# Performance work log

Measured on AMD Instinct MI355X. Metric: run time of the kernel, lower is better.

## Reference

```python
import math
import jax, jax.numpy as jnp
import numpy as np

NEG_INF = -jnp.inf


def setup_inputs() -> dict:
    key = jax.random.key(0)
    k1, k2, k3 = jax.random.split(key, 3)
    B, T, D = 2, 2048, 1024
    x = jax.random.normal(k1, (B, T, D), dtype=jnp.float32)
    w_qkv = jax.random.normal(k2, (3 * D, D), dtype=jnp.float32) * (1.0 / math.sqrt(D))
    w_out = jax.random.normal(k3, (D, D), dtype=jnp.float32) * (1.0 / math.sqrt(D))
    return {"x": x, "w_qkv": w_qkv, "w_out": w_out, "n_heads": 16, "k": 8}


def reference(x, w_qkv, w_out, n_heads, k):
    B, T, D = x.shape
    head_dim = D // n_heads
    scale = math.sqrt(head_dim)

    qkv = x @ w_qkv.T                                   # (B,T,3D), torch Linear: x W^T
    q, kk, v = jnp.split(qkv, 3, axis=-1)

    def split_heads(t):
        return t.reshape(B, T, n_heads, head_dim).transpose(0, 2, 1, 3)  # (B,H,T,dh)

    q, kk, v = split_heads(q), split_heads(kk), split_heads(v)

    scores = jnp.einsum("bhqd,bhkd->bhqk", q, kk) / scale  # (B,H,T,T)
    causal = jnp.tril(jnp.ones((T, T), dtype=bool))
    scores = jnp.where(causal, scores, NEG_INF)

    # per-row effective k: min(k, n_valid) with n_valid = row index + 1
    top_vals = jax.lax.top_k(scores, k)[0]                 # (B,H,T,k), sorted desc
    k_eff_idx = jnp.minimum(jnp.arange(1, T + 1), k) - 1   # (T,)
    thresh = jnp.take_along_axis(
        top_vals, k_eff_idx[None, None, :, None], axis=-1  # (B,H,T,1)
    )
    keep = scores >= thresh                                # ties kept, matching torch >=
    scores = jnp.where(keep, scores, NEG_INF)

    attn = jax.nn.softmax(scores, axis=-1)
    attn = jnp.nan_to_num(attn)                            # defensive; rows never all -inf
    out = jnp.einsum("bhqk,bhkd->bhqd", attn, v)
    out = out.transpose(0, 2, 1, 3).reshape(B, T, D)       # merge heads
    return out @ w_out.T
```

## Files before the change

### kernel.cpp

```cpp
#include <hip/hip_runtime.h>
#include <hip/hip_bf16.h>
#include <math.h>
#include <float.h>

#define NUM_B 2
#define SEQ_T 2048
#define DIM_D 1024
#define NH 16
#define DH 64
#define KDIM 1024
#define KSEL 8

#define CAP 32
#define MFMA_MARGIN 0.06f

typedef __attribute__((ext_vector_type(8))) short bf16x8v;
typedef __attribute__((ext_vector_type(4))) float f32x4v;
typedef __attribute__((ext_vector_type(4))) double f64x4v;

__device__ __forceinline__ float bf2f(unsigned int u) {
  union { unsigned int i; float f; } v; v.i = u << 16; return v.f;
}

__device__ __forceinline__ short f2bs(float f) {
  __hip_bfloat16 h = __float2bfloat16(f);
  return *(short*)&h;
}

__device__ __forceinline__ void split8(float4 x0, float4 x1,
                                       unsigned short* __restrict__ hp,
                                       unsigned short* __restrict__ lp) {
  unsigned short h[8], l[8];
  const float xs[8] = {x0.x, x0.y, x0.z, x0.w, x1.x, x1.y, x1.z, x1.w};
#pragma unroll
  for (int j = 0; j < 8; ++j) {
    const short hb = f2bs(xs[j]);
    h[j] = (unsigned short)hb;
    const float hf = bf2f((unsigned int)(unsigned short)hb);
    l[j] = (unsigned short)f2bs(xs[j] - hf);
  }
  *(uint4*)hp = *(const uint4*)h;
  *(uint4*)lp = *(const uint4*)l;
}

__device__ __forceinline__ void split4(float4 x,
                                       unsigned short* __restrict__ hp,
                                       unsigned short* __restrict__ lp) {
  unsigned short h[4], l[4];
  const float xs[4] = {x.x, x.y, x.z, x.w};
#pragma unroll
  for (int j = 0; j < 4; ++j) {
    const short hb = f2bs(xs[j]);
    h[j] = (unsigned short)hb;
    const float hf = bf2f((unsigned int)(unsigned short)hb);
    l[j] = (unsigned short)f2bs(xs[j] - hf);
  }
  *(uint2*)hp = *(const uint2*)h;
  *(uint2*)lp = *(const uint2*)l;
}

__global__ __launch_bounds__(512) void gemm_qk(
    const float* __restrict__ A, const float* __restrict__ Bm,
    float* __restrict__ qbuf, float* __restrict__ kbuf,
    unsigned short* __restrict__ kbf) {
  __shared__ __align__(16) float As[64][36];
  __shared__ __align__(16) float Bs[128][36];
  const int tid = threadIdx.x;
  const int lane = tid & 63;
  const int w = tid >> 6;
  const int row0 = blockIdx.y * 64;
  const int col0 = blockIdx.x * 128;
  const int lrA = tid >> 3;
  const int lkA = (tid & 7) << 2;
  const int lrB = tid >> 2;
  const int lkB = (tid & 3) << 3;
  const float* ap = A + (size_t)(row0 + lrA) * KDIM + lkA;
  const float* bp = Bm + (size_t)(col0 + lrB) * KDIM + lkB;
  const int wr = (w >> 2) << 5;
  const int wc = (w & 3) << 5;
  const int li = lane & 15;
  const int lk4 = lane >> 4;

  int rowof[4], colof[4];
  {
    f64x4v pr = {0.0, 0.0, 0.0, 0.0};
    f64x4v pc = {0.0, 0.0, 0.0, 0.0};
    const double vidx = (double)li;
    pr = __builtin_amdgcn_mfma_f64_16x16x4f64(vidx, 1.0, pr, 0, 0, 0);
    pc = __builtin_amdgcn_mfma_f64_16x16x4f64(1.0, vidx, pc, 0, 0, 0);
#pragma unroll
    for (int vj = 0; vj < 4; ++vj) {
      rowof[vj] = (int)(pr[vj] * 0.25 + 0.5);
      colof[vj] = (int)(pc[vj] * 0.25 + 0.5);
    }
  }

  f64x4v acc[2][2];
#pragma unroll
  for (int m = 0; m < 2; ++m)
#pragma unroll
    for (int n = 0; n < 2; ++n)
      acc[m][n] = (f64x4v){0.0, 0.0, 0.0, 0.0};

  float4 ra = *(const float4*)(ap);
  float4 rb0 = *(const float4*)(bp);
  float4 rb1 = *(const float4*)(bp + 4);
  for (int k0 = 0; k0 < KDIM; k0 += 32) {
    __syncthreads();
    *(float4*)&As[lrA][lkA] = ra;
    *(float4*)&Bs[lrB][lkB] = rb0;
    *(float4*)&Bs[lrB][lkB + 4] = rb1;
    if (k0 + 32 < KDIM) {
      ra = *(const float4*)(ap + k0 + 32);
      rb0 = *(const float4*)(bp + k0 + 32);
      rb1 = *(const float4*)(bp + k0 + 36);
    }
    __syncthreads();
#pragma unroll
    for (int ks = 0; ks < 32; ks += 4) {
      const int kk = ks + lk4;
      const double af0 = (double)As[wr + li][kk];
      const double af1 = (double)As[wr + 16 + li][kk];
      const double bf0 = (double)Bs[wc + li][kk];
      const double bf1 = (double)Bs[wc + 16 + li][kk];
      acc[0][0] = __builtin_amdgcn_mfma_f64_16x16x4f64(af0, bf0, acc[0][0], 0, 0, 0);
      acc[0][1] = __builtin_amdgcn_mfma_f64_16x16x4f64(af0, bf1, acc[0][1], 0, 0, 0);
      acc[1][0] = __builtin_amdgcn_mfma_f64_16x16x4f64(af1, bf0, acc[1][0], 0, 0, 0);
      acc[1][1] = __builtin_amdgcn_mfma_f64_16x16x4f64(af1, bf1, acc[1][1], 0, 0, 0);
    }
  }

  const int bb = row0 >> 11;
  const int t0 = row0 & 2047;
#pragma unroll
  for (int m = 0; m < 2; ++m)
#pragma unroll
    for (int n = 0; n < 2; ++n)
#pragma unroll
      for (int vj = 0; vj < 4; ++vj) {
        const int r = wr + 16 * m + rowof[vj];
        const int gc = col0 + wc + 16 * n + colof[vj];
        const int qi = gc >> 10;
        const int head = (gc & 1023) >> 6;
        const int d = gc & 63;
        const int t = t0 + r;
        const float fv = (float)acc[m][n][vj];
        float* dst = ((qi == 0) ? qbuf : kbuf) +
                     (size_t)(bb * NH + head) * SEQ_T * DH;
        dst[(size_t)t * DH + d] = fv;
        if (qi == 1) {
          unsigned short* kb = kbf + ((size_t)(bb * NH + head) << 17);
          const int key = t & 127;
          const int off =
              (((t >> 7) << 13) | (key << 6) | d) ^ ((key & 7) << 3);
          __hip_bfloat16 hb = __float2bfloat16(fv);
          kb[off] = *(unsigned short*)&hb;
        }
      }
}

__global__ __launch_bounds__(512) void gemm_v(
    const float* __restrict__ A, const float* __restrict__ Bm,
    unsigned short* __restrict__ vbuf) {
  __shared__ __align__(16) unsigned short Ah[64][40];
  __shared__ __align__(16) unsigned short Al[64][40];
  __shared__ __align__(16) unsigned short Bh[128][40];
  __shared__ __align__(16) unsigned short Bl[128][40];
  const int tid = threadIdx.x;
  const int lane = tid & 63;
  const int w = tid >> 6;
  const int row0 = blockIdx.y * 64;
  const int col0v = blockIdx.x * 128;
  const int lrA = tid >> 3;
  const int lkA = (tid & 7) << 2;
  const int lrB = tid >> 2;
  const int lkB = (tid & 3) << 3;
  const float* ap = A + (size_t)(row0 + lrA) * KDIM + lkA;
  const float* bp = Bm + (size_t)(col0v + lrB) * KDIM + lkB;
  const int wr = (w >> 2) << 5;
  const int wc = (w & 3) << 5;
  const int li = lane & 15;
  const int kA = (lane >> 4) << 3;

  f32x4v acc[2][2];
#pragma unroll
  for (int m = 0; m < 2; ++m)
#pragma unroll
    for (int n = 0; n < 2; ++n)
      acc[m][n] = (f32x4v){0.f, 0.f, 0.f, 0.f};

  float4 ra = *(const float4*)(ap);
  float4 rb0 = *(const float4*)(bp);
  float4 rb1 = *(const float4*)(bp + 4);
  for (int k0 = 0; k0 < KDIM; k0 += 32) {
    __syncthreads();
    split4(ra, &Ah[lrA][lkA], &Al[lrA][lkA]);
    split8(rb0, rb1, &Bh[lrB][lkB], &Bl[lrB][lkB]);
    if (k0 + 32 < KDIM) {
      ra = *(const float4*)(ap + k0 + 32);
      rb0 = *(const float4*)(bp + k0 + 32);
      rb1 = *(const float4*)(bp + k0 + 36);
    }
    __syncthreads();
    bf16x8v ah[2], al[2], bh[2], bl[2];
#pragma unroll
    for (int m = 0; m < 2; ++m) {
      ah[m] = *(const bf16x8v*)&Ah[wr + 16 * m + li][kA];
      al[m] = *(const bf16x8v*)&Al[wr + 16 * m + li][kA];
      bh[m] = *(const bf16x8v*)&Bh[wc + 16 * m + li][kA];
      bl[m] = *(const bf16x8v*)&Bl[wc + 16 * m + li][kA];
    }
#pragma unroll
    for (int m = 0; m < 2; ++m)
#pragma unroll
      for (int n = 0; n < 2; ++n) {
        acc[m][n] = __builtin_amdgcn_mfma_f32_16x16x32_bf16(ah[m], bh[n], acc[m][n], 0, 0, 0);
        acc[m][n] = __builtin_amdgcn_mfma_f32_16x16x32_bf16(ah[m], bl[n], acc[m][n], 0, 0, 0);
        acc[m][n] = __builtin_amdgcn_mfma_f32_16x16x32_bf16(al[m], bh[n], acc[m][n], 0, 0, 0);
      }
  }

  const int bb = row0 >> 11;
  const int t0 = row0 & 2047;
  const int r4 = (lane >> 4) << 2;
#pragma unroll
  for (int m = 0; m < 2; ++m)
#pragma unroll
    for (int n = 0; n < 2; ++n)
#pragma unroll
      for (int j = 0; j < 4; ++j) {
        const int t = t0 + wr + 16 * m + r4 + j;
        const int vcol = col0v + wc + 16 * n + li;
        const int head = vcol >> 6;
        const int d = vcol & 63;
        vbuf[(size_t)(bb * NH + head) * SEQ_T * DH + (size_t)t * DH + d] =
            (unsigned short)f2bs(acc[m][n][j]);
      }
}

__global__ __launch_bounds__(512) void attn_scan(
    const float* __restrict__ q, const unsigned short* __restrict__ kbf,
    short* __restrict__ gckey, int* __restrict__ gccnt) {
  __shared__ __align__(16) unsigned short kt[128 * 64];
  __shared__ __align__(16) short ckey[128][CAP];
  __shared__ int ccnt[128];

  const int tid = threadIdx.x;
  const int lane = tid & 63;
  const int w = tid >> 6;
  const int bh = blockIdx.x & 31;
  const int u = blockIdx.x >> 5;
  const int g = (u < 8) ? u : 23 - u;
  const int t0 = g << 7;
  const size_t kbase = (size_t)bh * SEQ_T * DH;
  const int wrow0 = t0 + (w << 4);
  const int kA = (lane >> 4) << 3;
  const int rbase = wrow0 + ((lane >> 4) << 2);

  bf16x8v qa0, qa1;
  {
    const float* qr = q + kbase + (size_t)(wrow0 + (lane & 15)) * DH;
    const float4 x0 = *(const float4*)(qr + kA);
    const float4 x1 = *(const float4*)(qr + kA + 4);
    const float4 y0 = *(const float4*)(qr + 32 + kA);
    const float4 y1 = *(const float4*)(qr + 32 + kA + 4);
    qa0[0] = f2bs(x0.x); qa0[1] = f2bs(x0.y);
    qa0[2] = f2bs(x0.z); qa0[3] = f2bs(x0.w);
    qa0[4] = f2bs(x1.x); qa0[5] = f2bs(x1.y);
    qa0[6] = f2bs(x1.z); qa0[7] = f2bs(x1.w);
    qa1[0] = f2bs(y0.x); qa1[1] = f2bs(y0.y);
    qa1[2] = f2bs(y0.z); qa1[3] = f2bs(y0.w);
    qa1[4] = f2bs(y1.x); qa1[5] = f2bs(y1.y);
    qa1[6] = f2bs(y1.z); qa1[7] = f2bs(y1.w);
  }

  const uint4* ksrc = (const uint4*)(kbf + ((size_t)bh << 17));
  const int nt = (t0 >> 7) + 1;
  const int wmax = wrow0 + 15;

  float tq[4][8];
#pragma unroll
  for (int j = 0; j < 4; ++j)
#pragma unroll
    for (int m = 0; m < 8; ++m) tq[j][m] = -FLT_MAX;

  for (int T = 0; T < nt; ++T) {
    if (T) __syncthreads();
    {
      const uint4* st = ksrc + (size_t)T * 1024;
      uint4* dv = (uint4*)kt;
#pragma unroll
      for (int i = 0; i < 2; ++i) dv[i * 512 + tid] = st[i * 512 + tid];
    }
    __syncthreads();
    const int glim0 = (wmax - (T << 7)) >> 4;
    const int glim = glim0 > 7 ? 7 : glim0;
    for (int gt = 0; gt <= glim; ++gt) {
      const int kk = (gt << 4) + (lane & 15);
      const int key = (T << 7) + kk;
      const int b0 = ((kk << 7) | (kA << 1)) ^ ((kk & 7) << 4);
      const int b1 = ((kk << 7) | ((32 + kA) << 1)) ^ ((kk & 7) << 4);
      const bf16x8v kb0 = *(const bf16x8v*)((const char*)kt + b0);
      const bf16x8v kb1 = *(const bf16x8v*)((const char*)kt + b1);
      f32x4v acc = {0.f, 0.f, 0.f, 0.f};
      acc = __builtin_amdgcn_mfma_f32_16x16x32_bf16(qa0, kb0, acc, 0, 0, 0);
      acc = __builtin_amdgcn_mfma_f32_16x16x32_bf16(qa1, kb1, acc, 0, 0, 0);
#pragma unroll
      for (int j = 0; j < 4; ++j) {
        float sc = acc[j] * 0.125f;
        sc = (key <= rbase + j) ? sc : -FLT_MAX;
        if (sc > tq[j][7]) {
          float s = sc;
#pragma unroll
          for (int m = 0; m < 8; ++m) {
            const float hi = fmaxf(tq[j][m], s);
            s = fminf(tq[j][m], s);
            tq[j][m] = hi;
          }
        }
      }
    }
  }

#pragma unroll
  for (int j = 0; j < 4; ++j) {
#pragma unroll
    for (int xm = 1; xm < 16; xm <<= 1) {
      float m[8];
#pragma unroll
      for (int i = 0; i < 8; ++i) {
        const float pb = __shfl_xor(tq[j][7 - i], xm);
        m[i] = fmaxf(tq[j][i], pb);
      }
#pragma unroll
      for (int d = 4; d >= 1; d >>= 1)
#pragma unroll
        for (int i = 0; i < 8; ++i)
          if ((i & d) == 0 && (i | d) < 8) {
            const float hi = fmaxf(m[i], m[i | d]);
            const float lo = fminf(m[i], m[i | d]);
            m[i] = hi;
            m[i | d] = lo;
          }
#pragma unroll
      for (int i = 0; i < 8; ++i) tq[j][i] = m[i];
    }
  }
  float thrj[4];
#pragma unroll
  for (int j = 0; j < 4; ++j) {
    const int kf = (rbase + j + 1 < KSEL) ? (rbase + j + 1) : KSEL;
    float th = tq[j][7];
#pragma unroll
    for (int m = 0; m < 8; ++m)
      if (m == kf - 1) th = tq[j][m];
    thrj[j] = th - MFMA_MARGIN;
  }

  if (tid < 128) ccnt[tid] = 0;
  __syncthreads();

  for (int T = 0; T < nt; ++T) {
    if (T) __syncthreads();
    {
      const uint4* st = ksrc + (size_t)T * 1024;
      uint4* dv = (uint4*)kt;
#pragma unroll
      for (int i = 0; i < 2; ++i) dv[i * 512 + tid] = st[i * 512 + tid];
    }
    __syncthreads();
    const int glim0 = (wmax - (T << 7)) >> 4;
    const int glim = glim0 > 7 ? 7 : glim0;
    for (int gt = 0; gt <= glim; ++gt) {
      const int kk = (gt << 4) + (lane & 15);
      const int key = (T << 7) + kk;
      const int b0 = ((kk << 7) | (kA << 1)) ^ ((kk & 7) << 4);
      const int b1 = ((kk << 7) | ((32 + kA) << 1)) ^ ((kk & 7) << 4);
      const bf16x8v kb0 = *(const bf16x8v*)((const char*)kt + b0);
      const bf16x8v kb1 = *(const bf16x8v*)((const char*)kt + b1);
      f32x4v acc = {0.f, 0.f, 0.f, 0.f};
      acc = __builtin_amdgcn_mfma_f32_16x16x32_bf16(qa0, kb0, acc, 0, 0, 0);
      acc = __builtin_amdgcn_mfma_f32_16x16x32_bf16(qa1, kb1, acc, 0, 0, 0);
#pragma unroll
      for (int j = 0; j < 4; ++j) {
        const float sc = acc[j] * 0.125f;
        if (key <= rbase + j && sc >= thrj[j]) {
          const int rl = (w << 4) + ((lane >> 4) << 2) + j;
          const int p = atomicAdd(&ccnt[rl], 1);
          if (p < CAP) ckey[rl][p] = (short)key;
        }
      }
    }
  }

  __syncthreads();
  {
    const int row = tid >> 2;
    const int sl = (tid & 3) << 3;
    *(uint4*)&gckey[((size_t)bh * SEQ_T + t0 + row) * CAP + sl] =
        *(const uint4*)&ckey[row][sl];
    if (tid < 128) gccnt[(size_t)bh * SEQ_T + t0 + tid] = ccnt[tid];
  }
}

__global__ __launch_bounds__(256) void attn_sel(
    const float* __restrict__ q, const float* __restrict__ kmat,
    const short* __restrict__ gckey, const int* __restrict__ gccnt,
    const unsigned short* __restrict__ v, unsigned short* __restrict__ ctx) {
  __shared__ __align__(16) double cs64[64][CAP];
  __shared__ __align__(16) short ckey[64][CAP];
  __shared__ int ccnt[64];
  __shared__ double rthr[64];
  __shared__ float rmx[64];

  const int tid = threadIdx.x;
  const int lane = tid & 63;
  const int w = tid >> 6;
  const int bh = blockIdx.x & 31;
  const int t0 = (blockIdx.x >> 5) << 6;
  const size_t kbase = (size_t)bh * SEQ_T * DH;

  {
    const int row = tid >> 2;
    const int sl = (tid & 3) << 3;
    *(uint4*)&ckey[row][sl] =
        *(const uint4*)&gckey[((size_t)bh * SEQ_T + t0 + row) * CAP + sl];
    if (tid < 64) ccnt[tid] = gccnt[(size_t)bh * SEQ_T + t0 + tid];
  }
  __syncthreads();

  const int lid = lane & 31;
  for (int rp = 0; rp < 8; ++rp) {
    const int rl = (w << 4) + (rp << 1) + (lane >> 5);
    const int ncc = ccnt[rl] < CAP ? ccnt[rl] : CAP;
    if (lid < ncc) {
      const int key = ckey[rl][lid];
      const float* qr = q + kbase + (size_t)(t0 + rl) * DH;
      const float* kr = kmat + kbase + (size_t)key * DH;
      double s = 0.0;
#pragma unroll
      for (int d4 = 0; d4 < 16; ++d4) {
        const float4 qq = *(const float4*)(qr + (d4 << 2));
        const float4 kq = *(const float4*)(kr + (d4 << 2));
        s = fma((double)qq.x, (double)kq.x, s);
        s = fma((double)qq.y, (double)kq.y, s);
        s = fma((double)qq.z, (double)kq.z, s);
        s = fma((double)qq.w, (double)kq.w, s);
      }
      cs64[rl][lid] = s * 0.125;
    }
  }
  __syncthreads();

  if (lane < 16) {
    const int rl = (w << 4) + lane;
    const int trow = t0 + rl;
    const int ncc = ccnt[rl] < CAP ? ccnt[rl] : CAP;
    double a64[8];
#pragma unroll
    for (int j = 0; j < 8; ++j) a64[j] = -DBL_MAX;
    for (int l = 0; l < ncc; ++l) {
      double sv = cs64[rl][l];
#pragma unroll
      for (int j = 0; j < 8; ++j) {
        const double hi = fmax(a64[j], sv);
        sv = fmin(a64[j], sv);
        a64[j] = hi;
      }
    }
    const int kf = (trow + 1 < KSEL) ? (trow + 1) : KSEL;
    double th = a64[7];
#pragma unroll
    for (int j = 0; j < 8; ++j)
      if (j == kf - 1) th = a64[j];
    rthr[rl] = th;
    rmx[rl] = (float)a64[0];
  }
  __syncthreads();

  for (int rg = 0; rg < 4; ++rg) {
    const int rlb = (w << 4) + (rg << 2);
    float acv[4] = {0.f, 0.f, 0.f, 0.f};
    float Zs[4] = {0.f, 0.f, 0.f, 0.f};
    int ncs[4];
    double ths[4];
    float mxs[4];
#pragma unroll
    for (int j = 0; j < 4; ++j) {
      const int rl = rlb + j;
      ncs[j] = ccnt[rl] < CAP ? ccnt[rl] : CAP;
      ths[j] = rthr[rl];
      mxs[j] = rmx[rl];
    }
    int nmax = ncs[0];
#pragma unroll
    for (int j = 1; j < 4; ++j) nmax = ncs[j] > nmax ? ncs[j] : nmax;
    for (int l = 0; l < nmax; ++l) {
#pragma unroll
      for (int j = 0; j < 4; ++j) {
        const int rl = rlb + j;
        if (l < ncs[j]) {
          const double s = cs64[rl][l];
          const float wgl = (s >= ths[j]) ? expf((float)s - mxs[j]) : 0.f;
          Zs[j] += wgl;
          acv[j] = fmaf(
              wgl,
              bf2f((unsigned int)v[kbase + (size_t)ckey[rl][l] * DH + lane]),
              acv[j]);
        }
      }
    }
#pragma unroll
    for (int j = 0; j < 4; ++j) {
      const int trow = t0 + rlb + j;
      __hip_bfloat16 h = __float2bfloat16(acv[j] / Zs[j]);
      ctx[((size_t)(bh >> 4) * SEQ_T + trow) * DIM_D + (bh & 15) * DH + lane] =
          *(unsigned short*)&h;
    }
  }
}

__global__ __launch_bounds__(256) void gemm_out(
    const unsigned short* __restrict__ A, const float* __restrict__ Bm,
    float* __restrict__ obuf) {
  __shared__ __align__(16) unsigned short Ah[64][40];
  __shared__ __align__(16) unsigned short Bh[64][40];
  __shared__ __align__(16) unsigned short Bl[64][40];
  const int tid = threadIdx.x;
  const int lane = tid & 63;
  const int w = tid >> 6;
  const int row0 = blockIdx.y * 64;
  const int col0 = blockIdx.x * 64;
  const int lrow = tid >> 2;
  const int lk = (tid & 3) << 3;
  const unsigned short* ap = A + (size_t)(row0 + lrow) * KDIM + lk;
  const float* bp = Bm + (size_t)(col0 + lrow) * KDIM + lk;
  const int wr = (w >> 1) << 5;
  const int wc = (w & 1) << 5;
  const int li = lane & 15;
  const int kA = (lane >> 4) << 3;

  f32x4v acc[2][2];
#pragma unroll
  for (int m = 0; m < 2; ++m)
#pragma unroll
    for (int n = 0; n < 2; ++n)
      acc[m][n] = (f32x4v){0.f, 0.f, 0.f, 0.f};

  uint4 ua = *(const uint4*)(ap);
  float4 rb0 = *(const float4*)(bp);
  float4 rb1 = *(const float4*)(bp + 4);
  for (int k0 = 0; k0 < KDIM; k0 += 32) {
    __syncthreads();
    *(uint4*)&Ah[lrow][lk] = ua;
    split8(rb0, rb1, &Bh[lrow][lk], &Bl[lrow][lk]);
    if (k0 + 32 < KDIM) {
      ua = *(const uint4*)(ap + k0 + 32);
      rb0 = *(const float4*)(bp + k0 + 32);
      rb1 = *(const float4*)(bp + k0 + 36);
    }
    __syncthreads();
    bf16x8v ah[2], bh[2], bl[2];
#pragma unroll
    for (int m = 0; m < 2; ++m) {
      ah[m] = *(const bf16x8v*)&Ah[wr + 16 * m + li][kA];
      bh[m] = *(const bf16x8v*)&Bh[wc + 16 * m + li][kA];
      bl[m] = *(const bf16x8v*)&Bl[wc + 16 * m + li][kA];
    }
#pragma unroll
    for (int m = 0; m < 2; ++m)
#pragma unroll
      for (int n = 0; n < 2; ++n) {
        acc[m][n] = __builtin_amdgcn_mfma_f32_16x16x32_bf16(ah[m], bh[n], acc[m][n], 0, 0, 0);
        acc[m][n] = __builtin_amdgcn_mfma_f32_16x16x32_bf16(ah[m], bl[n], acc[m][n], 0, 0, 0);
      }
  }

  const int r4 = (lane >> 4) << 2;
#pragma unroll
  for (int m = 0; m < 2; ++m)
#pragma unroll
    for (int n = 0; n < 2; ++n)
#pragma unroll
      for (int j = 0; j < 4; ++j) {
        const int r = row0 + wr + 16 * m + r4 + j;
        const int c = col0 + wc + 16 * n + li;
        obuf[(size_t)r * DIM_D + c] = acc[m][n][j];
      }
}

extern "C" void kernel_launch(void* const* d_in, const int* in_sizes, int n_in,
                              void* d_out, int out_size, void* d_ws,
                              size_t ws_size, hipStream_t stream) {
  (void)out_size; (void)ws_size;
  const float* x = (const float*)d_in[0];
  const float* wqkv = (const float*)d_in[1];
  const float* wout = (const float*)d_in[2];
  for (int i = 0; i < n_in; ++i) {
    if (in_sizes[i] == NUM_B * SEQ_T * DIM_D) x = (const float*)d_in[i];
    else if (in_sizes[i] == 3 * DIM_D * DIM_D) wqkv = (const float*)d_in[i];
    else if (in_sizes[i] == DIM_D * DIM_D) wout = (const float*)d_in[i];
  }
  float* out = (float*)d_out;

  const size_t qkv_elems = (size_t)NUM_B * NH * SEQ_T * DH;
  float* qbuf = (float*)d_ws;
  float* kbuf = qbuf + qkv_elems;
  unsigned short* vbuf = (unsigned short*)(kbuf + qkv_elems);
  unsigned short* ctxb = vbuf + qkv_elems;
  unsigned short* kbf = ctxb + (size_t)NUM_B * SEQ_T * DIM_D;
  short* gckey = (short*)(kbf + ((size_t)NUM_B * NH << 17));
  int* gccnt = (int*)(gckey + (size_t)NUM_B * NH * SEQ_T * CAP);

  gemm_qk<<<dim3(2 * DIM_D / 128, NUM_B * SEQ_T / 64), 512, 0, stream>>>(
      x, wqkv, qbuf, kbuf, kbf);
  gemm_v<<<dim3(DIM_D / 128, NUM_B * SEQ_T / 64), 512, 0, stream>>>(
      x, wqkv + (size_t)2 * DIM_D * KDIM, vbuf);
  attn_scan<<<dim3(NUM_B * NH * (SEQ_T / 128)), 512, 0, stream>>>(
      qbuf, kbf, gckey, gccnt);
  attn_sel<<<dim3(NUM_B * NH * (SEQ_T / 64)), 256, 0, stream>>>(
      qbuf, kbuf, gckey, gccnt, vbuf, ctxb);
  gemm_out<<<dim3(DIM_D / 64, NUM_B * SEQ_T / 64), 256, 0, stream>>>(
      ctxb, wout, out);
}
```

Measured before the change: 613.7 us.

## Split causal top-k scan into key-chunked partial, threshold merge, and collect kernels

```diff
diff --git a/kernel.cpp b/kernel.cpp
--- a/kernel.cpp
+++ b/kernel.cpp
@@ -57,6 +57,12 @@
   }
   *(uint2*)hp = *(const uint2*)h;
   *(uint2*)lp = *(const uint2*)l;
+}
+
+__device__ __forceinline__ int cum_chunks(int g) {
+  int cum = 0;
+  for (int h = 0; h < g; ++h) cum += (h >> 2) + 1;
+  return cum;
 }
 
 __global__ __launch_bounds__(512) void gemm_qk(
@@ -238,19 +244,24 @@
       }
 }
 
-__global__ __launch_bounds__(512) void attn_scan(
+__global__ __launch_bounds__(512) void attn_part(
     const float* __restrict__ q, const unsigned short* __restrict__ kbf,
-    short* __restrict__ gckey, int* __restrict__ gccnt) {
+    float* __restrict__ gpart) {
   __shared__ __align__(16) unsigned short kt[128 * 64];
-  __shared__ __align__(16) short ckey[128][CAP];
-  __shared__ int ccnt[128];
-
   const int tid = threadIdx.x;
   const int lane = tid & 63;
   const int w = tid >> 6;
   const int bh = blockIdx.x & 31;
-  const int u = blockIdx.x >> 5;
-  const int g = (u < 8) ? u : 23 - u;
+  const int r = blockIdx.x >> 5;
+  int g = 0, c = 0;
+  {
+    int cum = 0;
+    for (int h = 0; h < 16; ++h) {
+      const int ch = (h >> 2) + 1;
+      if (r >= cum && r < cum + ch) { g = h; c = r - cum; }
+      cum += ch;
+    }
+  }
   const int t0 = g << 7;
   const size_t kbase = (size_t)bh * SEQ_T * DH;
   const int wrow0 = t0 + (w << 4);
@@ -275,7 +286,9 @@
   }
 
   const uint4* ksrc = (const uint4*)(kbf + ((size_t)bh << 17));
-  const int nt = (t0 >> 7) + 1;
+  const int Tbeg = c << 2;
+  const int rem = (g + 1) - Tbeg;
+  const int Tcnt = rem < 4 ? rem : 4;
   const int wmax = wrow0 + 15;
 
   float tq[4][8];
@@ -284,8 +297,9 @@
 #pragma unroll
     for (int m = 0; m < 8; ++m) tq[j][m] = -FLT_MAX;
 
-  for (int T = 0; T < nt; ++T) {
-    if (T) __syncthreads();
+  for (int Ti = 0; Ti < Tcnt; ++Ti) {
+    const int T = Tbeg + Ti;
+    if (Ti) __syncthreads();
     {
       const uint4* st = ksrc + (size_t)T * 1024;
       uint4* dv = (uint4*)kt;
@@ -346,22 +360,109 @@
       for (int i = 0; i < 8; ++i) tq[j][i] = m[i];
     }
   }
-  float thrj[4];
-#pragma unroll
-  for (int j = 0; j < 4; ++j) {
-    const int kf = (rbase + j + 1 < KSEL) ? (rbase + j + 1) : KSEL;
-    float th = tq[j][7];
-#pragma unroll
-    for (int m = 0; m < 8; ++m)
-      if (m == kf - 1) th = tq[j][m];
-    thrj[j] = th - MFMA_MARGIN;
-  }
-
-  if (tid < 128) ccnt[tid] = 0;
-  __syncthreads();
-
-  for (int T = 0; T < nt; ++T) {
-    if (T) __syncthreads();
+
+  const int sl = lane & 15;
+  if (sl < 8) {
+#pragma unroll
+    for (int j = 0; j < 4; ++j) {
+      const int rl = (w << 4) + ((lane >> 4) << 2) + j;
+      gpart[((size_t)blockIdx.x * 128 + rl) * 8 + sl] = tq[j][sl];
+    }
+  }
+}
+
+__global__ __launch_bounds__(128) void attn_thr(
+    const float* __restrict__ gpart, float* __restrict__ gthr,
+    int* __restrict__ gccnt) {
+  const int bh = blockIdx.x & 31;
+  const int g = blockIdx.x >> 5;
+  const int rl = threadIdx.x;
+  const int t = (g << 7) + rl;
+  const int cum = cum_chunks(g);
+  const int nch = (g >> 2) + 1;
+  float a[8];
+#pragma unroll
+  for (int j = 0; j < 8; ++j) a[j] = -FLT_MAX;
+  for (int cc = 0; cc < nch; ++cc) {
+    const float* p =
+        gpart + (((size_t)(cum + cc) * 32 + bh) * 128 + rl) * 8;
+#pragma unroll
+    for (int i = 0; i < 8; ++i) {
+      float s = p[i];
+      if (s > a[7]) {
+#pragma unroll
+        for (int m = 0; m < 8; ++m) {
+          const float hi = fmaxf(a[m], s);
+          s = fminf(a[m], s);
+          a[m] = hi;
+        }
+      }
+    }
+  }
+  const int kf = (t + 1 < KSEL) ? (t + 1) : KSEL;
+  float th = a[7];
+#pragma unroll
+  for (int j = 0; j < 8; ++j)
+    if (j == kf - 1) th = a[j];
+  gthr[bh * SEQ_T + t] = th - MFMA_MARGIN;
+  gccnt[bh * SEQ_T + t] = 0;
+}
+
+__global__ __launch_bounds__(512) void attn_coll(
+    const float* __restrict__ q, const unsigned short* __restrict__ kbf,
+    const float* __restrict__ gthr, short* __restrict__ gckey,
+    int* __restrict__ gccnt) {
+  __shared__ __align__(16) unsigned short kt[128 * 64];
+  const int tid = threadIdx.x;
+  const int lane = tid & 63;
+  const int w = tid >> 6;
+  const int bh = blockIdx.x & 31;
+  const int r = blockIdx.x >> 5;
+  int g = 0, c = 0;
+  {
+    int cum = 0;
+    for (int h = 0; h < 16; ++h) {
+      const int ch = (h >> 2) + 1;
+      if (r >= cum && r < cum + ch) { g = h; c = r - cum; }
+      cum += ch;
+    }
+  }
+  const int t0 = g << 7;
+  const size_t kbase = (size_t)bh * SEQ_T * DH;
+  const int wrow0 = t0 + (w << 4);
+  const int kA = (lane >> 4) << 3;
+  const int rbase = wrow0 + ((lane >> 4) << 2);
+
+  bf16x8v qa0, qa1;
+  {
+    const float* qr = q + kbase + (size_t)(wrow0 + (lane & 15)) * DH;
+    const float4 x0 = *(const float4*)(qr + kA);
+    const float4 x1 = *(const float4*)(qr + kA + 4);
+    const float4 y0 = *(const float4*)(qr + 32 + kA);
+    const float4 y1 = *(const float4*)(qr + 32 + kA + 4);
+    qa0[0] = f2bs(x0.x); qa0[1] = f2bs(x0.y);
+    qa0[2] = f2bs(x0.z); qa0[3] = f2bs(x0.w);
+    qa0[4] = f2bs(x1.x); qa0[5] = f2bs(x1.y);
+    qa0[6] = f2bs(x1.z); qa0[7] = f2bs(x1.w);
+    qa1[0] = f2bs(y0.x); qa1[1] = f2bs(y0.y);
+    qa1[2] = f2bs(y0.z); qa1[3] = f2bs(y0.w);
+    qa1[4] = f2bs(y1.x); qa1[5] = f2bs(y1.y);
+    qa1[6] = f2bs(y1.z); qa1[7] = f2bs(y1.w);
+  }
+
+  float thj[4];
+#pragma unroll
+  for (int j = 0; j < 4; ++j) thj[j] = gthr[bh * SEQ_T + rbase + j];
+
+  const uint4* ksrc = (const uint4*)(kbf + ((size_t)bh << 17));
+  const int Tbeg = c << 2;
+  const int rem = (g + 1) - Tbeg;
+  const int Tcnt = rem < 4 ? rem : 4;
+  const int wmax = wrow0 + 15;
+
+  for (int Ti = 0; Ti < Tcnt; ++Ti) {
+    const int T = Tbeg + Ti;
+    if (Ti) __syncthreads();
     {
       const uint4* st = ksrc + (size_t)T * 1024;
       uint4* dv = (uint4*)kt;
@@ -384,22 +485,13 @@
 #pragma unroll
       for (int j = 0; j < 4; ++j) {
         const float sc = acc[j] * 0.125f;
-        if (key <= rbase + j && sc >= thrj[j]) {
-          const int rl = (w << 4) + ((lane >> 4) << 2) + j;
-          const int p = atomicAdd(&ccnt[rl], 1);
-          if (p < CAP) ckey[rl][p] = (short)key;
+        if (key <= rbase + j && sc >= thj[j]) {
+          const int trow = rbase + j;
+          const int p = atomicAdd(&gccnt[bh * SEQ_T + trow], 1);
+          if (p < CAP) gckey[((size_t)bh * SEQ_T + trow) * CAP + p] = (short)key;
         }
       }
     }
-  }
-
-  __syncthreads();
-  {
-    const int row = tid >> 2;
-    const int sl = (tid & 3) << 3;
-    *(uint4*)&gckey[((size_t)bh * SEQ_T + t0 + row) * CAP + sl] =
-        *(const uint4*)&ckey[row][sl];
-    if (tid < 128) gccnt[(size_t)bh * SEQ_T + t0 + tid] = ccnt[tid];
   }
 }
 
@@ -604,20 +696,24 @@
   float* out = (float*)d_out;
 
   const size_t qkv_elems = (size_t)NUM_B * NH * SEQ_T * DH;
+  const size_t nrows = (size_t)NUM_B * NH * SEQ_T;
   float* qbuf = (float*)d_ws;
   float* kbuf = qbuf + qkv_elems;
   unsigned short* vbuf = (unsigned short*)(kbuf + qkv_elems);
   unsigned short* ctxb = vbuf + qkv_elems;
   unsigned short* kbf = ctxb + (size_t)NUM_B * SEQ_T * DIM_D;
   short* gckey = (short*)(kbf + ((size_t)NUM_B * NH << 17));
-  int* gccnt = (int*)(gckey + (size_t)NUM_B * NH * SEQ_T * CAP);
+  int* gccnt = (int*)(gckey + nrows * CAP);
+  float* gpart = (float*)(gccnt + nrows);
+  float* gthr = gpart + (size_t)1280 * 128 * 8;
 
   gemm_qk<<<dim3(2 * DIM_D / 128, NUM_B * SEQ_T / 64), 512, 0, stream>>>(
       x, wqkv, qbuf, kbuf, kbf);
   gemm_v<<<dim3(DIM_D / 128, NUM_B * SEQ_T / 64), 512, 0, stream>>>(
       x, wqkv + (size_t)2 * DIM_D * KDIM, vbuf);
-  attn_scan<<<dim3(NUM_B * NH * (SEQ_T / 128)), 512, 0, stream>>>(
-      qbuf, kbf, gckey, gccnt);
+  attn_part<<<dim3(40 * 32), 512, 0, stream>>>(qbuf, kbf, gpart);
+  attn_thr<<<dim3(16 * 32), 128, 0, stream>>>(gpart, gthr, gccnt);
+  attn_coll<<<dim3(40 * 32), 512, 0, stream>>>(qbuf, kbf, gthr, gckey, gccnt);
   attn_sel<<<dim3(NUM_B * NH * (SEQ_T / 64)), 256, 0, stream>>>(
       qbuf, kbuf, gckey, gccnt, vbuf, ctxb);
   gemm_out<<<dim3(DIM_D / 64, NUM_B * SEQ_T / 64), 256, 0, stream>>>(
```

After: 644.4 us. 1.05x slower.
